# Optimization experiments

Measured on AMD Instinct MI355X. Metric: run time of the kernel, lower is better.

## Reference

```python
import jax, jax.numpy as jnp
import numpy as np

LEVELS = 3


def _wavelet_pyramid(x, levels=LEVELS):
    """Faithful jax port of WaveletTransform.forward.

    Per level: take top-left (H/2^l, W/2^l) region, convolve with the 3x3
    separable low-pass kernel outer([.25,.5,.25]) using zero-padded 'same'
    conv (kernel is symmetric so scipy's flip is a no-op), then write the
    2x-strided downsample into the top-left quarter.
    """
    B, C, H, W = x.shape
    k1 = jnp.array([0.25, 0.5, 0.25], dtype=x.dtype)
    K = jnp.outer(k1, k1)[None, None]  # [1,1,3,3] low_pass.T @ low_pass
    result = x
    for level in range(levels):
        sh, sw = H // (2 ** level), W // (2 ** level)
        if min(sh, sw) <= 2:
            break
        # fold B,C into batch: per-channel 2D conv, zero boundary = scipy 'same'
        temp = result[:, :, :sh, :sw].reshape(B * C, 1, sh, sw)
        approx = jax.lax.conv_general_dilated(
            temp, K, window_strides=(1, 1), padding='SAME',
            dimension_numbers=('NCHW', 'OIHW', 'NCHW'))
        down = approx[:, :, ::2, ::2][:, :, :sh // 2, :sw // 2]
        result = result.at[:, :, :sh // 2, :sw // 2].set(
            down.reshape(B, C, sh // 2, sw // 2))
    return result


def setup_inputs() -> dict:
    key = jax.random.key(0)
    x = jax.random.normal(key, (8, 32, 512, 512), dtype=jnp.float32)
    return {"x": x}


def reference(x):
    return _wavelet_pyramid(x, LEVELS)
```

## Files before the change

kernel.cpp:

```cpp
#include <hip/hip_runtime.h>

#define W 512
#define IMG (512 * 512)
#define NIMG 256
#define L1SZ (128 * 128)

__global__ __launch_bounds__(256) void kA(const float* __restrict__ x,
                                          float* __restrict__ out) {
    const int gid = blockIdx.x;
    const int img = gid >> 7;
    const int b   = gid & 127;
    const int tid = threadIdx.x;
    const int lane = tid & 63;
    const int i  = (b >> 1) * 4 + (tid >> 6);
    const int jq = (b & 1) * 64 + lane;
    const int c0 = 4 * jq;

    const float* xi = x + (size_t)img * IMG;
    float* oi = out + (size_t)img * IMG;
    const int r0 = 2 * i - 1, r1 = 2 * i, r2 = 2 * i + 1;

    float4 m1 = *(const float4*)(xi + r1 * W + c0);
    float4 m2 = *(const float4*)(xi + r2 * W + c0);
    float4 m0 = (r0 >= 0) ? *(const float4*)(xi + r0 * W + c0)
                          : make_float4(0.f, 0.f, 0.f, 0.f);

    float p0 = __shfl_up(m0.w, 1, 64);
    float p1 = __shfl_up(m1.w, 1, 64);
    float p2 = __shfl_up(m2.w, 1, 64);
    if (lane == 0) {
        if (c0 == 0) {
            p0 = p1 = p2 = 0.f;
        } else {
            p1 = xi[r1 * W + c0 - 1];
            p2 = xi[r2 * W + c0 - 1];
            p0 = (r0 >= 0) ? xi[r0 * W + c0 - 1] : 0.f;
        }
    }

    float ha0 = 0.25f * p0 + 0.5f * m0.x + 0.25f * m0.y;
    float hb0 = 0.25f * m0.y + 0.5f * m0.z + 0.25f * m0.w;
    float ha1 = 0.25f * p1 + 0.5f * m1.x + 0.25f * m1.y;
    float hb1 = 0.25f * m1.y + 0.5f * m1.z + 0.25f * m1.w;
    float ha2 = 0.25f * p2 + 0.5f * m2.x + 0.25f * m2.y;
    float hb2 = 0.25f * m2.y + 0.5f * m2.z + 0.25f * m2.w;
    float2 o;
    o.x = 0.25f * ha0 + 0.5f * ha1 + 0.25f * ha2;
    o.y = 0.25f * hb0 + 0.5f * hb1 + 0.25f * hb2;
    *(float2*)(oi + i * W + 2 * jq) = o;

    if (i >= 128 || jq >= 64) {
        *(float4*)(oi + r1 * W + c0) = m1;
        *(float4*)(oi + r2 * W + c0) = m2;
    }
}

__global__ __launch_bounds__(256) void kB(const float* __restrict__ out,
                                          float* __restrict__ ws) {
    const int gid = blockIdx.x;
    const int img = gid >> 5;
    const int b   = gid & 31;
    const int tid = threadIdx.x;
    const int lane = tid & 63;
    const int i  = b * 4 + (tid >> 6);
    const int c0 = 4 * lane;

    const float* oi = out + (size_t)img * IMG;
    float* wsi = ws + (size_t)img * L1SZ;
    const int r0 = 2 * i - 1, r1 = 2 * i, r2 = 2 * i + 1;

    float4 m1 = *(const float4*)(oi + r1 * W + c0);
    float4 m2 = *(const float4*)(oi + r2 * W + c0);
    float4 m0 = (r0 >= 0) ? *(const float4*)(oi + r0 * W + c0)
                          : make_float4(0.f, 0.f, 0.f, 0.f);
    float p0 = __shfl_up(m0.w, 1, 64);
    float p1 = __shfl_up(m1.w, 1, 64);
    float p2 = __shfl_up(m2.w, 1, 64);
    if (lane == 0) { p0 = p1 = p2 = 0.f; }

    float ha0 = 0.25f * p0 + 0.5f * m0.x + 0.25f * m0.y;
    float hb0 = 0.25f * m0.y + 0.5f * m0.z + 0.25f * m0.w;
    float ha1 = 0.25f * p1 + 0.5f * m1.x + 0.25f * m1.y;
    float hb1 = 0.25f * m1.y + 0.5f * m1.z + 0.25f * m1.w;
    float ha2 = 0.25f * p2 + 0.5f * m2.x + 0.25f * m2.y;
    float hb2 = 0.25f * m2.y + 0.5f * m2.z + 0.25f * m2.w;
    float2 o;
    o.x = 0.25f * ha0 + 0.5f * ha1 + 0.25f * ha2;
    o.y = 0.25f * hb0 + 0.5f * hb1 + 0.25f * hb2;
    *(float2*)(wsi + i * 128 + 2 * lane) = o;
}

__global__ __launch_bounds__(256) void kC(const float* __restrict__ ws,
                                          float* __restrict__ out) {
    const int gid = blockIdx.x;
    const int img = gid >> 3;
    const int b   = gid & 7;
    const int tid = threadIdx.x;
    const int i2  = b * 8 + (tid >> 5);
    const int jq2 = tid & 31;
    const int c0  = 4 * jq2;

    const float* wsi = ws + (size_t)img * L1SZ;
    float* oi = out + (size_t)img * IMG;
    const int r0 = 2 * i2 - 1, r1 = 2 * i2, r2 = 2 * i2 + 1;

    float4 m1 = *(const float4*)(wsi + r1 * 128 + c0);
    float4 m2 = *(const float4*)(wsi + r2 * 128 + c0);
    float4 m0 = (r0 >= 0) ? *(const float4*)(wsi + r0 * 128 + c0)
                          : make_float4(0.f, 0.f, 0.f, 0.f);
    float p0 = __shfl_up(m0.w, 1, 64);
    float p1 = __shfl_up(m1.w, 1, 64);
    float p2 = __shfl_up(m2.w, 1, 64);
    if (jq2 == 0) { p0 = p1 = p2 = 0.f; }

    float ha0 = 0.25f * p0 + 0.5f * m0.x + 0.25f * m0.y;
    float hb0 = 0.25f * m0.y + 0.5f * m0.z + 0.25f * m0.w;
    float ha1 = 0.25f * p1 + 0.5f * m1.x + 0.25f * m1.y;
    float hb1 = 0.25f * m1.y + 0.5f * m1.z + 0.25f * m1.w;
    float ha2 = 0.25f * p2 + 0.5f * m2.x + 0.25f * m2.y;
    float hb2 = 0.25f * m2.y + 0.5f * m2.z + 0.25f * m2.w;
    float2 o;
    o.x = 0.25f * ha0 + 0.5f * ha1 + 0.25f * ha2;
    o.y = 0.25f * hb0 + 0.5f * hb1 + 0.25f * hb2;
    *(float2*)(oi + i2 * W + 2 * jq2) = o;

    if (r1 >= 64 || c0 >= 64) {
        *(float4*)(oi + r1 * W + c0) = m1;
        *(float4*)(oi + r2 * W + c0) = m2;
    }
}

extern "C" void kernel_launch(void* const* d_in, const int* in_sizes, int n_in,
                              void* d_out, int out_size, void* d_ws,
                              size_t ws_size, hipStream_t stream) {
    const float* x = (const float*)d_in[0];
    float* out = (float*)d_out;
    float* ws = (float*)d_ws;
    (void)in_sizes; (void)n_in; (void)ws_size; (void)out_size;

    kA<<<NIMG * 128, 256, 0, stream>>>(x, out);
    kB<<<NIMG * 32, 256, 0, stream>>>(out, ws);
    kC<<<NIMG * 8, 256, 0, stream>>>(ws, out);
}
```

Measured before the change: 457.7 us.

## Fuse wavelet levels two and three into one per-image kernel using shared memory

Replaces the separate level-2 and level-3 kernels, which passed data through a global workspace, with one kernel per image that keeps the 128x128 level-2 result in padded LDS. After a block barrier it writes back the non-overlapping part and computes level 3 directly from shared memory. This removes a kernel launch and the workspace round-trip. In exchange only 256 blocks of 1024 threads run, with large LDS per block, which lowers parallelism.

```diff
diff --git a/kernel.cpp b/kernel.cpp
--- a/kernel.cpp
+++ b/kernel.cpp
@@ -3,7 +3,6 @@
 #define W 512
 #define IMG (512 * 512)
 #define NIMG 256
-#define L1SZ (128 * 128)
 
 __global__ __launch_bounds__(256) void kA(const float* __restrict__ x,
                                           float* __restrict__ out) {
@@ -55,78 +54,75 @@
     }
 }
 
-__global__ __launch_bounds__(256) void kB(const float* __restrict__ out,
-                                          float* __restrict__ ws) {
-    const int gid = blockIdx.x;
-    const int img = gid >> 5;
-    const int b   = gid & 31;
+#define S1P 132
+__global__ __launch_bounds__(1024) void kBC2(float* __restrict__ out) {
+    __shared__ float S1[128 * S1P];
+    const int img = blockIdx.x;
+    float* oi = out + (size_t)img * IMG;
     const int tid = threadIdx.x;
     const int lane = tid & 63;
-    const int i  = b * 4 + (tid >> 6);
-    const int c0 = 4 * lane;
+    const int wv = tid >> 6;
 
-    const float* oi = out + (size_t)img * IMG;
-    float* wsi = ws + (size_t)img * L1SZ;
-    const int r0 = 2 * i - 1, r1 = 2 * i, r2 = 2 * i + 1;
+    for (int k = 0; k < 8; ++k) {
+        const int i = wv + 16 * k;
+        const int r0 = 2 * i - 1, r1 = 2 * i, r2 = 2 * i + 1;
+        const int c0 = 4 * lane;
+        float4 m1 = *(const float4*)(oi + r1 * W + c0);
+        float4 m2 = *(const float4*)(oi + r2 * W + c0);
+        float4 m0 = (r0 >= 0) ? *(const float4*)(oi + r0 * W + c0)
+                              : make_float4(0.f, 0.f, 0.f, 0.f);
+        float p0 = __shfl_up(m0.w, 1, 64);
+        float p1 = __shfl_up(m1.w, 1, 64);
+        float p2 = __shfl_up(m2.w, 1, 64);
+        if (lane == 0) { p0 = p1 = p2 = 0.f; }
+        float ha0 = 0.25f * p0 + 0.5f * m0.x + 0.25f * m0.y;
+        float hb0 = 0.25f * m0.y + 0.5f * m0.z + 0.25f * m0.w;
+        float ha1 = 0.25f * p1 + 0.5f * m1.x + 0.25f * m1.y;
+        float hb1 = 0.25f * m1.y + 0.5f * m1.z + 0.25f * m1.w;
+        float ha2 = 0.25f * p2 + 0.5f * m2.x + 0.25f * m2.y;
+        float hb2 = 0.25f * m2.y + 0.5f * m2.z + 0.25f * m2.w;
+        float2 o;
+        o.x = 0.25f * ha0 + 0.5f * ha1 + 0.25f * ha2;
+        o.y = 0.25f * hb0 + 0.5f * hb1 + 0.25f * hb2;
+        *(float2*)(&S1[i * S1P + 2 * lane]) = o;
+    }
+    __syncthreads();
 
-    float4 m1 = *(const float4*)(oi + r1 * W + c0);
-    float4 m2 = *(const float4*)(oi + r2 * W + c0);
-    float4 m0 = (r0 >= 0) ? *(const float4*)(oi + r0 * W + c0)
-                          : make_float4(0.f, 0.f, 0.f, 0.f);
-    float p0 = __shfl_up(m0.w, 1, 64);
-    float p1 = __shfl_up(m1.w, 1, 64);
-    float p2 = __shfl_up(m2.w, 1, 64);
-    if (lane == 0) { p0 = p1 = p2 = 0.f; }
+    for (int k = 0; k < 4; ++k) {
+        const int idx = tid + 1024 * k;
+        const int row = idx >> 5;
+        const int cq  = (idx & 31) * 4;
+        if (row >= 64 || cq >= 64) {
+            *(float4*)(oi + row * W + cq) = *(const float4*)(&S1[row * S1P + cq]);
+        }
+    }
 
-    float ha0 = 0.25f * p0 + 0.5f * m0.x + 0.25f * m0.y;
-    float hb0 = 0.25f * m0.y + 0.5f * m0.z + 0.25f * m0.w;
-    float ha1 = 0.25f * p1 + 0.5f * m1.x + 0.25f * m1.y;
-    float hb1 = 0.25f * m1.y + 0.5f * m1.z + 0.25f * m1.w;
-    float ha2 = 0.25f * p2 + 0.5f * m2.x + 0.25f * m2.y;
-    float hb2 = 0.25f * m2.y + 0.5f * m2.z + 0.25f * m2.w;
-    float2 o;
-    o.x = 0.25f * ha0 + 0.5f * ha1 + 0.25f * ha2;
-    o.y = 0.25f * hb0 + 0.5f * hb1 + 0.25f * hb2;
-    *(float2*)(wsi + i * 128 + 2 * lane) = o;
-}
-
-__global__ __launch_bounds__(256) void kC(const float* __restrict__ ws,
-                                          float* __restrict__ out) {
-    const int gid = blockIdx.x;
-    const int img = gid >> 3;
-    const int b   = gid & 7;
-    const int tid = threadIdx.x;
-    const int i2  = b * 8 + (tid >> 5);
-    const int jq2 = tid & 31;
-    const int c0  = 4 * jq2;
-
-    const float* wsi = ws + (size_t)img * L1SZ;
-    float* oi = out + (size_t)img * IMG;
-    const int r0 = 2 * i2 - 1, r1 = 2 * i2, r2 = 2 * i2 + 1;
-
-    float4 m1 = *(const float4*)(wsi + r1 * 128 + c0);
-    float4 m2 = *(const float4*)(wsi + r2 * 128 + c0);
-    float4 m0 = (r0 >= 0) ? *(const float4*)(wsi + r0 * 128 + c0)
-                          : make_float4(0.f, 0.f, 0.f, 0.f);
-    float p0 = __shfl_up(m0.w, 1, 64);
-    float p1 = __shfl_up(m1.w, 1, 64);
-    float p2 = __shfl_up(m2.w, 1, 64);
-    if (jq2 == 0) { p0 = p1 = p2 = 0.f; }
-
-    float ha0 = 0.25f * p0 + 0.5f * m0.x + 0.25f * m0.y;
-    float hb0 = 0.25f * m0.y + 0.5f * m0.z + 0.25f * m0.w;
-    float ha1 = 0.25f * p1 + 0.5f * m1.x + 0.25f * m1.y;
-    float hb1 = 0.25f * m1.y + 0.5f * m1.z + 0.25f * m1.w;
-    float ha2 = 0.25f * p2 + 0.5f * m2.x + 0.25f * m2.y;
-    float hb2 = 0.25f * m2.y + 0.5f * m2.z + 0.25f * m2.w;
-    float2 o;
-    o.x = 0.25f * ha0 + 0.5f * ha1 + 0.25f * ha2;
-    o.y = 0.25f * hb0 + 0.5f * hb1 + 0.25f * hb2;
-    *(float2*)(oi + i2 * W + 2 * jq2) = o;
-
-    if (r1 >= 64 || c0 >= 64) {
-        *(float4*)(oi + r1 * W + c0) = m1;
-        *(float4*)(oi + r2 * W + c0) = m2;
+    {
+        const int r  = tid >> 4;
+        const int cb = (tid & 15) * 8;
+        const int r0 = 2 * r - 1, r1 = 2 * r, r2 = 2 * r + 1;
+        float h[3][4];
+        for (int s = 0; s < 3; ++s) {
+            const int rr = (s == 0) ? r0 : (s == 1) ? r1 : r2;
+            if (rr < 0) {
+                h[s][0] = h[s][1] = h[s][2] = h[s][3] = 0.f;
+            } else {
+                const float* Sr = &S1[rr * S1P];
+                float left = (cb == 0) ? 0.f : Sr[cb - 1];
+                #pragma unroll
+                for (int q = 0; q < 4; ++q) {
+                    const int c = cb + 2 * q;
+                    float a = (q == 0) ? left : Sr[c - 1];
+                    h[s][q] = 0.25f * a + 0.5f * Sr[c] + 0.25f * Sr[c + 1];
+                }
+            }
+        }
+        float4 o;
+        o.x = 0.25f * h[0][0] + 0.5f * h[1][0] + 0.25f * h[2][0];
+        o.y = 0.25f * h[0][1] + 0.5f * h[1][1] + 0.25f * h[2][1];
+        o.z = 0.25f * h[0][2] + 0.5f * h[1][2] + 0.25f * h[2][2];
+        o.w = 0.25f * h[0][3] + 0.5f * h[1][3] + 0.25f * h[2][3];
+        *(float4*)(oi + r * W + (tid & 15) * 4) = o;
     }
 }
 
@@ -135,10 +131,8 @@
                               size_t ws_size, hipStream_t stream) {
     const float* x = (const float*)d_in[0];
     float* out = (float*)d_out;
-    float* ws = (float*)d_ws;
-    (void)in_sizes; (void)n_in; (void)ws_size; (void)out_size;
+    (void)in_sizes; (void)n_in; (void)d_ws; (void)ws_size; (void)out_size;
 
     kA<<<NIMG * 128, 256, 0, stream>>>(x, out);
-    kB<<<NIMG * 32, 256, 0, stream>>>(out, ws);
-    kC<<<NIMG * 8, 256, 0, stream>>>(ws, out);
+    kBC2<<<NIMG, 1024, 0, stream>>>(out);
 }
```

Result: no change. 449.3 us (-1.8%).
